# Kernel tuning notes

Measured on AMD Instinct MI355X. Metric: run time of the kernel, lower is better.

## Reference

```python
import jax, jax.numpy as jnp
import numpy as np

D_MODEL = 1024
NHEAD = 16
HEAD_DIM = D_MODEL // NHEAD
SF_THRESHOLD = 4.0
SF_LEVELS = 8
SF_STEP = SF_THRESHOLD / SF_LEVELS  # 0.5
EPS = 1e-6


def sfn(x):
    # Scale-and-Fire neuron: quantize activations to multiples of SF_STEP,
    # clipped to +/- num_levels, with straight-through estimator.
    q = jnp.clip(jnp.round(x / SF_STEP), -SF_LEVELS, SF_LEVELS) * SF_STEP
    return x + jax.lax.stop_gradient(q - x)


def qk_norm(x, g):
    # RMS-normalize over the head_dim (last axis) with learnable gain g [Dh].
    rms = jnp.sqrt(jnp.mean(x * x, axis=-1, keepdims=True) + EPS)
    return (x / rms) * g


def setup_inputs() -> dict:
    key = jax.random.key(0)
    ks = jax.random.split(key, 10)
    B, L, D = 2, 2048, D_MODEL
    s = 1.0 / np.sqrt(D)
    return {
        "x": jax.random.normal(ks[0], (B, L, D), dtype=jnp.float32),
        "Wq": jax.random.normal(ks[1], (D, D), dtype=jnp.float32) * s,
        "bq": jnp.zeros((D,), dtype=jnp.float32),
        "Wk": jax.random.normal(ks[2], (D, D), dtype=jnp.float32) * s,
        "bk": jnp.zeros((D,), dtype=jnp.float32),
        "Wv": jax.random.normal(ks[3], (D, D), dtype=jnp.float32) * s,
        "bv": jnp.zeros((D,), dtype=jnp.float32),
        "Wo": jax.random.normal(ks[4], (D, D), dtype=jnp.float32) * s,
        "bo": jnp.zeros((D,), dtype=jnp.float32),
        "gq": jnp.ones((HEAD_DIM,), dtype=jnp.float32),
        "gk": jnp.ones((HEAD_DIM,), dtype=jnp.float32),
    }


def reference(x, Wq, bq, Wk, bk, Wv, bv, Wo, bo, gq, gk):
    B, L, D = x.shape
    H, Dh = NHEAD, HEAD_DIM
    scale = Dh ** (-0.5)

    q = sfn(x @ Wq.T + bq)
    k = sfn(x @ Wk.T + bk)
    v = sfn(x @ Wv.T + bv)

    # [B, L, H, Dh] -> [B, H, L, Dh]
    q = q.reshape(B, L, H, Dh).transpose(0, 2, 1, 3)
    k = k.reshape(B, L, H, Dh).transpose(0, 2, 1, 3)
    v = v.reshape(B, L, H, Dh).transpose(0, 2, 1, 3)

    q = qk_norm(q, gq)
    k = qk_norm(k, gk)

    scores = jnp.einsum('bhqd,bhkd->bhqk', q, k) * scale
    probs = jax.nn.softmax(scores, axis=-1)  # dropout is identity (eval)
    out = jnp.einsum('bhqk,bhkd->bhqd', probs, v)
    out = out.transpose(0, 2, 1, 3).reshape(B, L, D)
    return out @ Wo.T + bo
```

## Files before the change

### kernel.cpp

```cpp
#include <hip/hip_runtime.h>
#include <math.h>


typedef __bf16 bf16;
typedef bf16 bf16x4 __attribute__((ext_vector_type(4)));
typedef bf16 bf16x8 __attribute__((ext_vector_type(8)));
typedef float f32x4 __attribute__((ext_vector_type(4)));

#define LOG2E 1.4426950408889634f
#define MFMA16 __builtin_amdgcn_mfma_f32_16x16x32_bf16
#define S_WAITV(N) asm volatile("s_waitcnt vmcnt(" #N ")" ::: "memory")

__device__ __forceinline__ void bar() {
  asm volatile("" ::: "memory");
  __builtin_amdgcn_s_barrier();
  asm volatile("" ::: "memory");
}

__device__ __forceinline__ float sfn_f(float x) {
  return fminf(fmaxf(rintf(x + x), -8.0f), 8.0f) * 0.5f;
}

__device__ __forceinline__ void gload16(const bf16* g, bf16* l) {
  __builtin_amdgcn_global_load_lds((const __attribute__((address_space(1))) void*)g,
                                   (__attribute__((address_space(3))) void*)l, 16, 0, 0);
}


__global__ __launch_bounds__(256) void prep_x_kernel(const float* __restrict__ x,
                                                     bf16* __restrict__ ax) {
  int idx = blockIdx.x * 256 + threadIdx.x;
  int m  = idx >> 8;
  int kc = (idx & 255) << 2;
  const float4 v = *(const float4*)(x + (size_t)m * 1024 + kc);
  bf16 h0 = (bf16)v.x, h1 = (bf16)v.y, h2 = (bf16)v.z, h3 = (bf16)v.w;
  bf16 l0 = (bf16)(v.x - (float)h0), l1 = (bf16)(v.y - (float)h1),
       l2 = (bf16)(v.z - (float)h2), l3 = (bf16)(v.w - (float)h3);
  bf16x4 hv = {h0, h1, h2, h3};
  bf16x4 lv = {l0, l1, l2, l3};
  bf16* p = ax + (size_t)m * 3072 + kc;
  *(bf16x4*)(p)        = hv;
  *(bf16x4*)(p + 1024) = lv;
  *(bf16x4*)(p + 2048) = hv;
}

__global__ __launch_bounds__(256) void prep_w_kernel(const float* __restrict__ Wq,
                                                     const float* __restrict__ Wk,
                                                     const float* __restrict__ Wv,
                                                     bf16* __restrict__ wc) {
  int idx = blockIdx.x * 256 + threadIdx.x;
  int mat = idx >> 18;
  int r   = idx & 262143;
  int n   = r >> 8;
  int kc  = (r & 255) << 2;
  const float* W = (mat == 0) ? Wq : ((mat == 1) ? Wk : Wv);
  const float4 v = *(const float4*)(W + (size_t)n * 1024 + kc);
  bf16 h0 = (bf16)v.x, h1 = (bf16)v.y, h2 = (bf16)v.z, h3 = (bf16)v.w;
  bf16 l0 = (bf16)(v.x - (float)h0), l1 = (bf16)(v.y - (float)h1),
       l2 = (bf16)(v.z - (float)h2), l3 = (bf16)(v.w - (float)h3);
  bf16x4 hv = {h0, h1, h2, h3};
  bf16x4 lv = {l0, l1, l2, l3};
  bf16* p = wc + (size_t)(mat * 1024 + n) * 3072 + kc;
  *(bf16x4*)(p)        = hv;
  *(bf16x4*)(p + 1024) = hv;
  *(bf16x4*)(p + 2048) = lv;
}

__global__ __launch_bounds__(256) void prep_wo_kernel(const float* __restrict__ Wo,
                                                      bf16* __restrict__ wob) {
  int idx = blockIdx.x * 256 + threadIdx.x;
  const float4 v = *(const float4*)(Wo + (size_t)idx * 4);
  bf16x4 hv = {(bf16)v.x, (bf16)v.y, (bf16)v.z, (bf16)v.w};
  *(bf16x4*)(wob + (size_t)idx * 4) = hv;
}


__global__ __launch_bounds__(512, 2) void gemm_qkv_kernel(
    const bf16* __restrict__ A, const bf16* __restrict__ Bm,
    const float* __restrict__ b0, const float* __restrict__ b1,
    const float* __restrict__ b2, const float* __restrict__ g0,
    const float* __restrict__ g1, bf16* __restrict__ qn, bf16* __restrict__ kn,
    bf16* __restrict__ vt) {
  constexpr int K = 3072, NT = 48;
  __shared__ bf16 lds[2][4][128 * 64];
  const int tid  = threadIdx.x;
  const int wave = tid >> 6;
  const int lane = tid & 63;
  const int lm   = lane & 15;
  const int kg   = lane >> 4;
  const int wm   = wave >> 2;
  const int wn   = wave & 3;
  const int lid     = blockIdx.x;
  const int logical = (lid & 7) * 24 + (lid >> 3);
  const int m0 = (logical / 12) << 8;
  const int n0 = (logical % 12) << 8;

  const bf16* Abase = A  + (size_t)m0 * K;
  const bf16* Bbase = Bm + (size_t)n0 * K;

  auto stageHalf = [&](int buf, int half, const bf16* base, int kt) {
#pragma unroll
    for (int j = 0; j < 2; ++j) {
      const int c    = j * 512 + tid;
      const int row  = c >> 3;
      const int col8 = (c & 7) ^ (row & 7);
      gload16(base + (size_t)row * K + kt + col8 * 8, &lds[buf][half][c * 8]);
    }
  };

  f32x4 acc[8][4] = {};
  const int bHalf = 2 + (wn >> 1);
  const int bRow  = (wn & 1) << 6;
  const int sw    = lm & 7;

  stageHalf(0, 0, Abase, 0);
  stageHalf(0, 1, Abase + (size_t)128 * K, 0);
  stageHalf(0, 2, Bbase, 0);
  stageHalf(0, 3, Bbase + (size_t)128 * K, 0);
  stageHalf(1, 0, Abase, 64);
  stageHalf(1, 1, Abase + (size_t)128 * K, 64);
  S_WAITV(4);
  bar();

  for (int t = 0; t < NT; ++t) {
    const int cur = t & 1, nxt = cur ^ 1;
    const int kt1 = (t + 1) << 6;
    bf16x8 a[4][2], p01[2][2], p23[2][2];
#pragma unroll
    for (int r = 0; r < 4; ++r)
#pragma unroll
      for (int kk = 0; kk < 2; ++kk)
        a[r][kk] = *(const bf16x8*)&lds[cur][wm][(16 * r + lm) * 64 + (((kk << 2) + kg) ^ sw) * 8];
#pragma unroll
    for (int c = 0; c < 2; ++c)
#pragma unroll
      for (int kk = 0; kk < 2; ++kk)
        p01[c][kk] = *(const bf16x8*)&lds[cur][bHalf][(bRow + 16 * c + lm) * 64 + (((kk << 2) + kg) ^ sw) * 8];
    if (t + 1 < NT) stageHalf(nxt, 2, Bbase, kt1);
    bar();
    __builtin_amdgcn_s_setprio(1);
#pragma unroll
    for (int r = 0; r < 4; ++r)
#pragma unroll
      for (int c = 0; c < 2; ++c)
#pragma unroll
        for (int kk = 0; kk < 2; ++kk)
          acc[r][c] = MFMA16(a[r][kk], p01[c][kk], acc[r][c], 0, 0, 0);
    __builtin_amdgcn_s_setprio(0);
    bar();
#pragma unroll
    for (int c = 0; c < 2; ++c)
#pragma unroll
      for (int kk = 0; kk < 2; ++kk)
        p23[c][kk] = *(const bf16x8*)&lds[cur][bHalf][(bRow + 16 * (c + 2) + lm) * 64 + (((kk << 2) + kg) ^ sw) * 8];
    if (t + 1 < NT) stageHalf(nxt, 3, Bbase + (size_t)128 * K, kt1);
    bar();
    __builtin_amdgcn_s_setprio(1);
#pragma unroll
    for (int r = 0; r < 4; ++r)
#pragma unroll
      for (int c = 0; c < 2; ++c)
#pragma unroll
        for (int kk = 0; kk < 2; ++kk)
          acc[r][c + 2] = MFMA16(a[r][kk], p23[c][kk], acc[r][c + 2], 0, 0, 0);
    __builtin_amdgcn_s_setprio(0);
    bar();
#pragma unroll
    for (int r = 0; r < 4; ++r)
#pragma unroll
      for (int kk = 0; kk < 2; ++kk)
        a[r][kk] = *(const bf16x8*)&lds[cur][wm][(64 + 16 * r + lm) * 64 + (((kk << 2) + kg) ^ sw) * 8];
    bar();
    __builtin_amdgcn_s_setprio(1);
#pragma unroll
    for (int r = 0; r < 4; ++r)
#pragma unroll
      for (int c = 0; c < 2; ++c)
#pragma unroll
        for (int kk = 0; kk < 2; ++kk)
          acc[4 + r][c + 2] = MFMA16(a[r][kk], p23[c][kk], acc[4 + r][c + 2], 0, 0, 0);
    __builtin_amdgcn_s_setprio(0);
    bar();
    if (t + 2 < NT) {
      const int kt2 = (t + 2) << 6;
      stageHalf(cur, 0, Abase, kt2);
      stageHalf(cur, 1, Abase + (size_t)128 * K, kt2);
      S_WAITV(4);
    } else {
      S_WAITV(0);
    }
    bar();
    __builtin_amdgcn_s_setprio(1);
#pragma unroll
    for (int r = 0; r < 4; ++r)
#pragma unroll
      for (int c = 0; c < 2; ++c)
#pragma unroll
        for (int kk = 0; kk < 2; ++kk)
          acc[4 + r][c] = MFMA16(a[r][kk], p01[c][kk], acc[4 + r][c], 0, 0, 0);
    __builtin_amdgcn_s_setprio(0);
    bar();
  }

  const int ncb = n0 + (wn << 6);
  const int mat = ncb >> 10;
  const int nin = ncb & 1023;
  const int hh  = nin >> 6;
  const float* bias = (mat == 0) ? b0 : ((mat == 1) ? b1 : b2);
  float bvals[4];
#pragma unroll
  for (int c = 0; c < 4; ++c) bvals[c] = bias[nin + 16 * c + lm];

  if (mat < 2) {
    const float* gain = (mat == 0) ? g0 : g1;
    bf16* dst = (mat == 0) ? qn : kn;
    float gv[4];
#pragma unroll
    for (int c = 0; c < 4; ++c) gv[c] = gain[16 * c + lm];
#pragma unroll
    for (int r = 0; r < 8; ++r) {
      float y[4][4];
      float ss[4] = {0.f, 0.f, 0.f, 0.f};
#pragma unroll
      for (int c = 0; c < 4; ++c)
#pragma unroll
        for (int g = 0; g < 4; ++g) {
          float tq = sfn_f(acc[r][c][g] + bvals[c]);
          y[c][g] = tq;
          ss[g] += tq * tq;
        }
#pragma unroll
      for (int g = 0; g < 4; ++g) {
        float s = ss[g];
        s += __shfl_xor(s, 1);
        s += __shfl_xor(s, 2);
        s += __shfl_xor(s, 4);
        s += __shfl_xor(s, 8);
        ss[g] = 1.0f / sqrtf(s * (1.0f / 64.0f) + 1e-6f);
      }
      const int mbase = m0 + (wm << 7) + 16 * r + 4 * kg;
      const int bb = mbase >> 11;
      const int ll = mbase & 2047;
#pragma unroll
      for (int g = 0; g < 4; ++g) {
        bf16* rowp = dst + ((size_t)(bb * 16 + hh) * 2048 + (ll + g)) * 64;
#pragma unroll
        for (int c = 0; c < 4; ++c)
          rowp[16 * c + lm] = (bf16)(y[c][g] * ss[g] * gv[c]);
      }
    }
  } else {
#pragma unroll
    for (int r = 0; r < 8; ++r) {
      const int mbase = m0 + (wm << 7) + 16 * r + 4 * kg;
      const int bb = mbase >> 11;
      const int ll = mbase & 2047;
#pragma unroll
      for (int c = 0; c < 4; ++c) {
        bf16x4 pk;
#pragma unroll
        for (int g = 0; g < 4; ++g)
          pk[g] = (bf16)sfn_f(acc[r][c][g] + bvals[c]);
        *(bf16x4*)(vt + ((size_t)(bb * 16 + hh) * 64 + 16 * c + lm) * 2048 + ll) = pk;
      }
    }
  }
}


__global__ __launch_bounds__(256, 3) void gemm_o_kernel(
    const bf16* __restrict__ A, const bf16* __restrict__ Bm, int K,
    const float* __restrict__ b0, float* __restrict__ outf) {
  __shared__ bf16 sA[128 * 32];
  __shared__ bf16 sB[128 * 32];
  const int tid  = threadIdx.x;
  const int wave = tid >> 6;
  const int lane = tid & 63;
  const int lm   = lane & 15;
  const int kg   = lane >> 4;
  const int nbx = gridDim.x;
  const int lid = blockIdx.x + nbx * blockIdx.y;
  const int cpx = (nbx << 5) >> 3;
  const int logical = (lid & 7) * cpx + (lid >> 3);
  const int m0 = (logical / nbx) << 7;
  const int n0 = (logical % nbx) << 7;
  const int wm = (wave >> 1) << 6;
  const int wn = (wave & 1) << 6;

  f32x4 acc[4][4] = {};

  for (int kt = 0; kt < K; kt += 32) {
    __syncthreads();
#pragma unroll
    for (int j = 0; j < 2; ++j) {
      const int i   = wave * 128 + j * 64 + lane;
      const int row = i >> 2;
      const int kc  = (i & 3) << 3;
      gload16(A  + (size_t)(m0 + row) * K + kt + kc, sA + i * 8);
      gload16(Bm + (size_t)(n0 + row) * K + kt + kc, sB + i * 8);
    }
    __syncthreads();
    bf16x8 af[4], bfv[4];
#pragma unroll
    for (int r = 0; r < 4; ++r)
      af[r] = *(const bf16x8*)(sA + (wm + 16 * r + lm) * 32 + kg * 8);
#pragma unroll
    for (int c = 0; c < 4; ++c)
      bfv[c] = *(const bf16x8*)(sB + (wn + 16 * c + lm) * 32 + kg * 8);
#pragma unroll
    for (int r = 0; r < 4; ++r)
#pragma unroll
      for (int c = 0; c < 4; ++c)
        acc[r][c] = MFMA16(af[r], bfv[c], acc[r][c], 0, 0, 0);
  }

  float bvals[4];
#pragma unroll
  for (int c = 0; c < 4; ++c) bvals[c] = b0[n0 + wn + 16 * c + lm];
#pragma unroll
  for (int r = 0; r < 4; ++r) {
    const int mr = m0 + wm + 16 * r + 4 * kg;
#pragma unroll
    for (int c = 0; c < 4; ++c) {
      const int nc = n0 + wn + 16 * c + lm;
#pragma unroll
      for (int g = 0; g < 4; ++g)
        outf[(size_t)(mr + g) * 1024 + nc] = acc[r][c][g] + bvals[c];
    }
  }
}


__global__ __launch_bounds__(256, 3) void attn_kernel(const bf16* __restrict__ qn,
                                                      const bf16* __restrict__ kn,
                                                      const bf16* __restrict__ vt,
                                                      bf16* __restrict__ ao) {
  __shared__ bf16 sK[2][64 * 64];
  __shared__ bf16 sV[2][64 * 64];
  __shared__ bf16 sP[4][2][16 * 72];
  const int tid  = threadIdx.x;
  const int wave = tid >> 6;
  const int lane = tid & 63;
  const int lm   = lane & 15;
  const int kg   = lane >> 4;
  const int lid     = blockIdx.x + (blockIdx.y << 4);
  const int logical = ((lid & 7) << 6) | (lid >> 3);
  const int qblk    = logical & 15;
  const int bh      = logical >> 4;
  const int q0      = (qblk << 7) + (wave << 5);
  const bf16* qb = qn + (size_t)bh * 2048 * 64;
  const bf16* kb = kn + (size_t)bh * 2048 * 64;
  const bf16* vb = vt + (size_t)bh * 64 * 2048;

  const float C1 = 0.125f * LOG2E;
  const float C2 = -8.0f * LOG2E;

  const int srow7 = lane >> 3;
  const int scl   = (lane & 7) ^ srow7;
  auto stageK = [&](int buf, int kt) {
#pragma unroll
    for (int j = 0; j < 2; ++j) {
      const int ci  = wave * 2 + j;
      const int row = ci * 8 + srow7;
      gload16(kb + (size_t)(kt + row) * 64 + scl * 8, &sK[buf][ci * 512]);
    }
  };
  auto stageV = [&](int buf, int kt) {
#pragma unroll
    for (int j = 0; j < 2; ++j) {
      const int ci  = wave * 2 + j;
      const int row = ci * 8 + srow7;
      gload16(vb + (size_t)row * 2048 + kt + scl * 8, &sV[buf][ci * 512]);
    }
  };

  bf16x8 qf[2][2];
#pragma unroll
  for (int c = 0; c < 2; ++c)
#pragma unroll
    for (int dh = 0; dh < 2; ++dh)
      qf[c][dh] = *(const bf16x8*)(qb + (size_t)(q0 + 16 * c + lm) * 64 + dh * 32 + kg * 8);

  f32x4 o[4][2] = {};
  float lrun[2] = {0.f, 0.f};

  stageK(0, 0);
  stageV(0, 0);
  S_WAITV(0);
  bar();

  const int a7 = lm & 7;
  for (int t = 0; t < 32; ++t) {
    const int cur = t & 1, nxt = cur ^ 1;
    const int ktn = (t + 1) << 6;
    if (t < 31) stageK(nxt, ktn);

    bf16x8 ka[4][2];
#pragma unroll
    for (int rb = 0; rb < 4; ++rb)
#pragma unroll
      for (int dh = 0; dh < 2; ++dh)
        ka[rb][dh] = *(const bf16x8*)(&sK[cur][(16 * rb + lm) * 64 + ((dh * 4 + kg) ^ a7) * 8]);

    f32x4 s[4][2] = {};
    __builtin_amdgcn_s_setprio(1);
#pragma unroll
    for (int rb = 0; rb < 4; ++rb)
#pragma unroll
      for (int c = 0; c < 2; ++c)
#pragma unroll
        for (int dh = 0; dh < 2; ++dh)
          s[rb][c] = MFMA16(ka[rb][dh], qf[c][dh], s[rb][c], 0, 0, 0);
    __builtin_amdgcn_s_setprio(0);

    if (t < 31) stageV(nxt, ktn);

#pragma unroll
    for (int c = 0; c < 2; ++c)
#pragma unroll
      for (int rb = 0; rb < 4; ++rb) {
        bf16x4 pk;
#pragma unroll
        for (int g = 0; g < 4; ++g) {
          float p = __builtin_amdgcn_exp2f(fmaf(s[rb][c][g], C1, C2));
          lrun[c] += p;
          pk[g] = (bf16)p;
        }
        *(bf16x4*)(&sP[wave][c][lm * 72 + 16 * rb + 4 * kg]) = pk;
      }
    bf16x8 pb[2][2];
#pragma unroll
    for (int c = 0; c < 2; ++c)
#pragma unroll
      for (int kh = 0; kh < 2; ++kh)
        pb[c][kh] = *(const bf16x8*)(&sP[wave][c][lm * 72 + kh * 32 + kg * 8]);

    if (t < 31) { S_WAITV(4); } else { S_WAITV(0); }
    bar();

    bf16x8 va[4][2];
#pragma unroll
    for (int rbd = 0; rbd < 4; ++rbd)
#pragma unroll
      for (int kh = 0; kh < 2; ++kh)
        va[rbd][kh] = *(const bf16x8*)(&sV[cur][(16 * rbd + lm) * 64 + ((kh * 4 + kg) ^ a7) * 8]);

    __builtin_amdgcn_s_setprio(1);
#pragma unroll
    for (int rbd = 0; rbd < 4; ++rbd)
#pragma unroll
      for (int c = 0; c < 2; ++c)
#pragma unroll
        for (int kh = 0; kh < 2; ++kh)
          o[rbd][c] = MFMA16(va[rbd][kh], pb[c][kh], o[rbd][c], 0, 0, 0);
    __builtin_amdgcn_s_setprio(0);

    if (t < 31) {
      S_WAITV(2);
      bar();
    }
  }

  const int bb = bh >> 4;
  const int hh = bh & 15;
#pragma unroll
  for (int c = 0; c < 2; ++c) {
    float l = lrun[c];
    l += __shfl_xor(l, 16);
    l += __shfl_xor(l, 32);
    const float inv = 1.0f / l;
    const int q = q0 + 16 * c + lm;
    bf16* rowp = ao + (size_t)(bb * 2048 + q) * 1024 + hh * 64;
#pragma unroll
    for (int rbd = 0; rbd < 4; ++rbd) {
      bf16x4 pk;
#pragma unroll
      for (int g = 0; g < 4; ++g)
        pk[g] = (bf16)(o[rbd][c][g] * inv);
      *(bf16x4*)(rowp + 16 * rbd + 4 * kg) = pk;
    }
  }
}


extern "C" void kernel_launch(void* const* d_in, const int* in_sizes, int n_in,
                              void* d_out, int out_size, void* d_ws, size_t ws_size,
                              hipStream_t stream) {
  const float* x  = (const float*)d_in[0];
  const float* Wq = (const float*)d_in[1];
  const float* bq = (const float*)d_in[2];
  const float* Wk = (const float*)d_in[3];
  const float* bk = (const float*)d_in[4];
  const float* Wv = (const float*)d_in[5];
  const float* bv = (const float*)d_in[6];
  const float* Wo = (const float*)d_in[7];
  const float* bo = (const float*)d_in[8];
  const float* gq = (const float*)d_in[9];
  const float* gk = (const float*)d_in[10];
  float* out = (float*)d_out;

  char* ws = (char*)d_ws;
  bf16* ax   = (bf16*)(ws);
  bf16* wc   = (bf16*)(ws + 25165824);
  bf16* wob  = (bf16*)(ws + 44040192);
  bf16* qn   = (bf16*)(ws + 46137344);
  bf16* kn   = (bf16*)(ws + 54525952);
  bf16* vt   = (bf16*)(ws + 62914560);
  bf16* attn = (bf16*)(ws + 71303168);

  prep_x_kernel<<<dim3(4096), dim3(256), 0, stream>>>(x, ax);
  prep_w_kernel<<<dim3(3072), dim3(256), 0, stream>>>(Wq, Wk, Wv, wc);
  prep_wo_kernel<<<dim3(1024), dim3(256), 0, stream>>>(Wo, wob);

  gemm_qkv_kernel<<<dim3(192), dim3(512), 0, stream>>>(
      ax, wc, bq, bk, bv, gq, gk, qn, kn, vt);

  attn_kernel<<<dim3(16, 32), dim3(256), 0, stream>>>(qn, kn, vt, attn);

  gemm_o_kernel<<<dim3(8, 32), dim3(256), 0, stream>>>(
      attn, wob, 1024, bo, out);
}
```

Baseline: 260.4 us.

## Retile QKV GEMM to 256x192 over 256 blocks and software-pipeline attention QK/PV

The QKV projection GEMM moves from 256x256 tiles on 192 blocks to 256x192 tiles on 256 blocks. Each wave now owns 32 rows by 192 columns, and the LDS staging and the fused epilogue are restructured to match. The goal is better CU occupancy on the 256-CU part without a partial last wave of blocks. The attention kernel is software-pipelined: the QK^T scores for tile t+1 are computed while the PV MFMAs for tile t run. K uses triple buffering and there is one barrier per iteration. The changes cost more registers and more complex scheduling, plus a per-wave P buffer that relies on lgkmcnt waits for ordering.

Measured after the change: 247.6 us. 1.05x faster.

```diff
diff --git a/kernel.cpp b/kernel.cpp
--- a/kernel.cpp
+++ b/kernel.cpp
@@ -82,109 +82,106 @@
     const float* __restrict__ g1, bf16* __restrict__ qn, bf16* __restrict__ kn,
     bf16* __restrict__ vt) {
   constexpr int K = 3072, NT = 48;
-  __shared__ bf16 lds[2][4][128 * 64];
+  __shared__ bf16 lds[2][28672];
   const int tid  = threadIdx.x;
   const int wave = tid >> 6;
   const int lane = tid & 63;
   const int lm   = lane & 15;
   const int kg   = lane >> 4;
-  const int wm   = wave >> 2;
-  const int wn   = wave & 3;
   const int lid     = blockIdx.x;
-  const int logical = (lid & 7) * 24 + (lid >> 3);
-  const int m0 = (logical / 12) << 8;
-  const int n0 = (logical % 12) << 8;
-
-  const bf16* Abase = A  + (size_t)m0 * K;
-  const bf16* Bbase = Bm + (size_t)n0 * K;
-
-  auto stageHalf = [&](int buf, int half, const bf16* base, int kt) {
+  const int logical = ((lid & 7) << 5) | (lid >> 3);
+  const int m0 = (logical >> 4) << 8;
+  const int n0 = (logical & 15) * 192;
+
+  auto stageA = [&](int buf, int half, int kt) {
 #pragma unroll
     for (int j = 0; j < 2; ++j) {
       const int c    = j * 512 + tid;
       const int row  = c >> 3;
       const int col8 = (c & 7) ^ (row & 7);
-      gload16(base + (size_t)row * K + kt + col8 * 8, &lds[buf][half][c * 8]);
+      gload16(A + (size_t)(m0 + half * 128 + row) * K + kt + col8 * 8,
+              &lds[buf][half * 8192 + c * 8]);
     }
   };
-
-  f32x4 acc[8][4] = {};
-  const int bHalf = 2 + (wn >> 1);
-  const int bRow  = (wn & 1) << 6;
+  auto stageB = [&](int buf, int ch, int kt) {
+    const int row  = tid >> 3;
+    const int col8 = (tid & 7) ^ (row & 7);
+    gload16(Bm + (size_t)(n0 + ch * 64 + row) * K + kt + col8 * 8,
+            &lds[buf][16384 + ch * 4096 + tid * 8]);
+  };
+
   const int sw    = lm & 7;
-
-  stageHalf(0, 0, Abase, 0);
-  stageHalf(0, 1, Abase + (size_t)128 * K, 0);
-  stageHalf(0, 2, Bbase, 0);
-  stageHalf(0, 3, Bbase + (size_t)128 * K, 0);
-  stageHalf(1, 0, Abase, 64);
-  stageHalf(1, 1, Abase + (size_t)128 * K, 64);
+  const int arow  = (wave << 5) + lm;
+  auto rdA = [&](int buf, int r, int kk) -> bf16x8 {
+    const int row = arow + 16 * r;
+    return *(const bf16x8*)&lds[buf][(row >> 7) * 8192 + (row & 127) * 64 +
+                                     (((kk << 2) + kg) ^ sw) * 8];
+  };
+  auto rdB = [&](int buf, int c, int kk) -> bf16x8 {
+    const int col = 16 * c + lm;
+    return *(const bf16x8*)&lds[buf][16384 + (col >> 6) * 4096 + (col & 63) * 64 +
+                                     (((kk << 2) + kg) ^ sw) * 8];
+  };
+
+  f32x4 acc[2][12] = {};
+
+  stageA(0, 0, 0); stageA(0, 1, 0);
+  stageB(0, 0, 0); stageB(0, 1, 0); stageB(0, 2, 0);
+  stageA(1, 0, 64); stageA(1, 1, 64);
   S_WAITV(4);
   bar();
 
   for (int t = 0; t < NT; ++t) {
     const int cur = t & 1, nxt = cur ^ 1;
-    const int kt1 = (t + 1) << 6;
-    bf16x8 a[4][2], p01[2][2], p23[2][2];
-#pragma unroll
-    for (int r = 0; r < 4; ++r)
+    const int kt1 = (t + 1) << 6, kt2 = (t + 2) << 6;
+    bf16x8 a[2][2], bv[6];
+#pragma unroll
+    for (int r = 0; r < 2; ++r)
 #pragma unroll
       for (int kk = 0; kk < 2; ++kk)
-        a[r][kk] = *(const bf16x8*)&lds[cur][wm][(16 * r + lm) * 64 + (((kk << 2) + kg) ^ sw) * 8];
-#pragma unroll
-    for (int c = 0; c < 2; ++c)
-#pragma unroll
-      for (int kk = 0; kk < 2; ++kk)
-        p01[c][kk] = *(const bf16x8*)&lds[cur][bHalf][(bRow + 16 * c + lm) * 64 + (((kk << 2) + kg) ^ sw) * 8];
-    if (t + 1 < NT) stageHalf(nxt, 2, Bbase, kt1);
+        a[r][kk] = rdA(cur, r, kk);
+#pragma unroll
+    for (int c = 0; c < 6; ++c) bv[c] = rdB(cur, c, 0);
+    if (t + 1 < NT) stageB(nxt, 0, kt1);
     bar();
     __builtin_amdgcn_s_setprio(1);
 #pragma unroll
-    for (int r = 0; r < 4; ++r)
-#pragma unroll
-      for (int c = 0; c < 2; ++c)
-#pragma unroll
-        for (int kk = 0; kk < 2; ++kk)
-          acc[r][c] = MFMA16(a[r][kk], p01[c][kk], acc[r][c], 0, 0, 0);
+    for (int r = 0; r < 2; ++r)
+#pragma unroll
+      for (int c = 0; c < 6; ++c)
+        acc[r][c] = MFMA16(a[r][0], bv[c], acc[r][c], 0, 0, 0);
     __builtin_amdgcn_s_setprio(0);
     bar();
-#pragma unroll
-    for (int c = 0; c < 2; ++c)
-#pragma unroll
-      for (int kk = 0; kk < 2; ++kk)
-        p23[c][kk] = *(const bf16x8*)&lds[cur][bHalf][(bRow + 16 * (c + 2) + lm) * 64 + (((kk << 2) + kg) ^ sw) * 8];
-    if (t + 1 < NT) stageHalf(nxt, 3, Bbase + (size_t)128 * K, kt1);
+    bf16x8 bw[6];
+#pragma unroll
+    for (int c = 0; c < 6; ++c) bw[c] = rdB(cur, c + 6, 0);
+    if (t + 1 < NT) { stageB(nxt, 1, kt1); stageB(nxt, 2, kt1); }
     bar();
     __builtin_amdgcn_s_setprio(1);
 #pragma unroll
-    for (int r = 0; r < 4; ++r)
-#pragma unroll
-      for (int c = 0; c < 2; ++c)
-#pragma unroll
-        for (int kk = 0; kk < 2; ++kk)
-          acc[r][c + 2] = MFMA16(a[r][kk], p23[c][kk], acc[r][c + 2], 0, 0, 0);
+    for (int r = 0; r < 2; ++r)
+#pragma unroll
+      for (int c = 0; c < 6; ++c)
+        acc[r][c + 6] = MFMA16(a[r][0], bw[c], acc[r][c + 6], 0, 0, 0);
     __builtin_amdgcn_s_setprio(0);
     bar();
-#pragma unroll
-    for (int r = 0; r < 4; ++r)
-#pragma unroll
-      for (int kk = 0; kk < 2; ++kk)
-        a[r][kk] = *(const bf16x8*)&lds[cur][wm][(64 + 16 * r + lm) * 64 + (((kk << 2) + kg) ^ sw) * 8];
+    bf16x8 bx[6];
+#pragma unroll
+    for (int c = 0; c < 6; ++c) bx[c] = rdB(cur, c, 1);
     bar();
     __builtin_amdgcn_s_setprio(1);
 #pragma unroll
-    for (int r = 0; r < 4; ++r)
-#pragma unroll
-      for (int c = 0; c < 2; ++c)
-#pragma unroll
-        for (int kk = 0; kk < 2; ++kk)
-          acc[4 + r][c + 2] = MFMA16(a[r][kk], p23[c][kk], acc[4 + r][c + 2], 0, 0, 0);
+    for (int r = 0; r < 2; ++r)
+#pragma unroll
+      for (int c = 0; c < 6; ++c)
+        acc[r][c] = MFMA16(a[r][1], bx[c], acc[r][c], 0, 0, 0);
     __builtin_amdgcn_s_setprio(0);
     bar();
+    bf16x8 by[6];
+#pragma unroll
+    for (int c = 0; c < 6; ++c) by[c] = rdB(cur, c + 6, 1);
     if (t + 2 < NT) {
-      const int kt2 = (t + 2) << 6;
-      stageHalf(cur, 0, Abase, kt2);
-      stageHalf(cur, 1, Abase + (size_t)128 * K, kt2);
+      stageA(cur, 0, kt2); stageA(cur, 1, kt2);
       S_WAITV(4);
     } else {
       S_WAITV(0);
@@ -192,76 +189,77 @@
     bar();
     __builtin_amdgcn_s_setprio(1);
 #pragma unroll
-    for (int r = 0; r < 4; ++r)
-#pragma unroll
-      for (int c = 0; c < 2; ++c)
-#pragma unroll
-        for (int kk = 0; kk < 2; ++kk)
-          acc[4 + r][c] = MFMA16(a[r][kk], p01[c][kk], acc[4 + r][c], 0, 0, 0);
+    for (int r = 0; r < 2; ++r)
+#pragma unroll
+      for (int c = 0; c < 6; ++c)
+        acc[r][c + 6] = MFMA16(a[r][1], by[c], acc[r][c + 6], 0, 0, 0);
     __builtin_amdgcn_s_setprio(0);
     bar();
   }
 
-  const int ncb = n0 + (wn << 6);
-  const int mat = ncb >> 10;
-  const int nin = ncb & 1023;
-  const int hh  = nin >> 6;
-  const float* bias = (mat == 0) ? b0 : ((mat == 1) ? b1 : b2);
-  float bvals[4];
-#pragma unroll
-  for (int c = 0; c < 4; ++c) bvals[c] = bias[nin + 16 * c + lm];
-
-  if (mat < 2) {
-    const float* gain = (mat == 0) ? g0 : g1;
-    bf16* dst = (mat == 0) ? qn : kn;
-    float gv[4];
-#pragma unroll
-    for (int c = 0; c < 4; ++c) gv[c] = gain[16 * c + lm];
-#pragma unroll
-    for (int r = 0; r < 8; ++r) {
-      float y[4][4];
-      float ss[4] = {0.f, 0.f, 0.f, 0.f};
-#pragma unroll
-      for (int c = 0; c < 4; ++c)
+#pragma unroll
+  for (int h = 0; h < 3; ++h) {
+    const int gcol = n0 + (h << 6);
+    const int mat  = gcol >> 10;
+    const int cb   = gcol & 1023;
+    const int hh   = cb >> 6;
+    const float* bias = (mat == 0) ? b0 : ((mat == 1) ? b1 : b2);
+    float bvals[4];
+#pragma unroll
+    for (int j = 0; j < 4; ++j) bvals[j] = bias[cb + 16 * j + lm];
+
+    if (mat < 2) {
+      const float* gain = (mat == 0) ? g0 : g1;
+      bf16* dst = (mat == 0) ? qn : kn;
+      float gv[4];
+#pragma unroll
+      for (int j = 0; j < 4; ++j) gv[j] = gain[16 * j + lm];
+#pragma unroll
+      for (int r = 0; r < 2; ++r) {
+        float y[4][4];
+        float ss[4] = {0.f, 0.f, 0.f, 0.f};
+#pragma unroll
+        for (int j = 0; j < 4; ++j)
+#pragma unroll
+          for (int g = 0; g < 4; ++g) {
+            float tq = sfn_f(acc[r][4 * h + j][g] + bvals[j]);
+            y[j][g] = tq;
+            ss[g] += tq * tq;
+          }
 #pragma unroll
         for (int g = 0; g < 4; ++g) {
-          float tq = sfn_f(acc[r][c][g] + bvals[c]);
-          y[c][g] = tq;
-          ss[g] += tq * tq;
+          float s = ss[g];
+          s += __shfl_xor(s, 1);
+          s += __shfl_xor(s, 2);
+          s += __shfl_xor(s, 4);
+          s += __shfl_xor(s, 8);
+          ss[g] = 1.0f / sqrtf(s * (1.0f / 64.0f) + 1e-6f);
         }
-#pragma unroll
-      for (int g = 0; g < 4; ++g) {
-        float s = ss[g];
-        s += __shfl_xor(s, 1);
-        s += __shfl_xor(s, 2);
-        s += __shfl_xor(s, 4);
-        s += __shfl_xor(s, 8);
-        ss[g] = 1.0f / sqrtf(s * (1.0f / 64.0f) + 1e-6f);
+        const int mbase = m0 + (wave << 5) + 16 * r + 4 * kg;
+        const int bb = mbase >> 11;
+        const int ll = mbase & 2047;
+#pragma unroll
+        for (int g = 0; g < 4; ++g) {
+          bf16* rowp = dst + ((size_t)(bb * 16 + hh) * 2048 + (ll + g)) * 64;
+#pragma unroll
+          for (int j = 0; j < 4; ++j)
+            rowp[16 * j + lm] = (bf16)(y[j][g] * ss[g] * gv[j]);
+        }
       }
-      const int mbase = m0 + (wm << 7) + 16 * r + 4 * kg;
-      const int bb = mbase >> 11;
-      const int ll = mbase & 2047;
-#pragma unroll
-      for (int g = 0; g < 4; ++g) {
-        bf16* rowp = dst + ((size_t)(bb * 16 + hh) * 2048 + (ll + g)) * 64;
-#pragma unroll
-        for (int c = 0; c < 4; ++c)
-          rowp[16 * c + lm] = (bf16)(y[c][g] * ss[g] * gv[c]);
-      }
-    }
-  } else {
-#pragma unroll
-    for (int r = 0; r < 8; ++r) {
-      const int mbase = m0 + (wm << 7) + 16 * r + 4 * kg;
-      const int bb = mbase >> 11;
-      const int ll = mbase & 2047;
-#pragma unroll
-      for (int c = 0; c < 4; ++c) {
-        bf16x4 pk;
-#pragma unroll
-        for (int g = 0; g < 4; ++g)
-          pk[g] = (bf16)sfn_f(acc[r][c][g] + bvals[c]);
-        *(bf16x4*)(vt + ((size_t)(bb * 16 + hh) * 64 + 16 * c + lm) * 2048 + ll) = pk;
+    } else {
+#pragma unroll
+      for (int r = 0; r < 2; ++r) {
+        const int mbase = m0 + (wave << 5) + 16 * r + 4 * kg;
+        const int bb = mbase >> 11;
+        const int ll = mbase & 2047;
+#pragma unroll
+        for (int j = 0; j < 4; ++j) {
+          bf16x4 pk;
+#pragma unroll
+          for (int g = 0; g < 4; ++g)
+            pk[g] = (bf16)sfn_f(acc[r][4 * h + j][g] + bvals[j]);
+          *(bf16x4*)(vt + ((size_t)(bb * 16 + hh) * 64 + 16 * j + lm) * 2048 + ll) = pk;
+        }
       }
     }
   }
@@ -335,9 +333,9 @@
                                                       const bf16* __restrict__ kn,
                                                       const bf16* __restrict__ vt,
                                                       bf16* __restrict__ ao) {
-  __shared__ bf16 sK[2][64 * 64];
+  __shared__ bf16 sK[3][64 * 64];
   __shared__ bf16 sV[2][64 * 64];
-  __shared__ bf16 sP[4][2][16 * 72];
+  __shared__ bf16 sP[4][16 * 72];
   const int tid  = threadIdx.x;
   const int wave = tid >> 6;
   const int lane = tid & 63;
@@ -383,27 +381,22 @@
 
   f32x4 o[4][2] = {};
   float lrun[2] = {0.f, 0.f};
-
+  bf16x8 pb[2][2];
+  const int a7 = lm & 7;
+
+  stageV(0, 0);
   stageK(0, 0);
-  stageV(0, 0);
+  stageK(1, 64);
   S_WAITV(0);
   bar();
-
-  const int a7 = lm & 7;
-  for (int t = 0; t < 32; ++t) {
-    const int cur = t & 1, nxt = cur ^ 1;
-    const int ktn = (t + 1) << 6;
-    if (t < 31) stageK(nxt, ktn);
-
+  {
     bf16x8 ka[4][2];
 #pragma unroll
     for (int rb = 0; rb < 4; ++rb)
 #pragma unroll
       for (int dh = 0; dh < 2; ++dh)
-        ka[rb][dh] = *(const bf16x8*)(&sK[cur][(16 * rb + lm) * 64 + ((dh * 4 + kg) ^ a7) * 8]);
-
+        ka[rb][dh] = *(const bf16x8*)(&sK[0][(16 * rb + lm) * 64 + ((dh * 4 + kg) ^ a7) * 8]);
     f32x4 s[4][2] = {};
-    __builtin_amdgcn_s_setprio(1);
 #pragma unroll
     for (int rb = 0; rb < 4; ++rb)
 #pragma unroll
@@ -411,12 +404,8 @@
 #pragma unroll
         for (int dh = 0; dh < 2; ++dh)
           s[rb][c] = MFMA16(ka[rb][dh], qf[c][dh], s[rb][c], 0, 0, 0);
-    __builtin_amdgcn_s_setprio(0);
-
-    if (t < 31) stageV(nxt, ktn);
-
-#pragma unroll
-    for (int c = 0; c < 2; ++c)
+#pragma unroll
+    for (int c = 0; c < 2; ++c) {
 #pragma unroll
       for (int rb = 0; rb < 4; ++rb) {
         bf16x4 pk;
@@ -426,39 +415,88 @@
           lrun[c] += p;
           pk[g] = (bf16)p;
         }
-        *(bf16x4*)(&sP[wave][c][lm * 72 + 16 * rb + 4 * kg]) = pk;
+        *(bf16x4*)(&sP[wave][lm * 72 + 16 * rb + 4 * kg]) = pk;
       }
-    bf16x8 pb[2][2];
-#pragma unroll
-    for (int c = 0; c < 2; ++c)
+      asm volatile("s_waitcnt lgkmcnt(0)" ::: "memory");
 #pragma unroll
       for (int kh = 0; kh < 2; ++kh)
-        pb[c][kh] = *(const bf16x8*)(&sP[wave][c][lm * 72 + kh * 32 + kg * 8]);
-
-    if (t < 31) { S_WAITV(4); } else { S_WAITV(0); }
-    bar();
-
-    bf16x8 va[4][2];
-#pragma unroll
-    for (int rbd = 0; rbd < 4; ++rbd)
-#pragma unroll
-      for (int kh = 0; kh < 2; ++kh)
-        va[rbd][kh] = *(const bf16x8*)(&sV[cur][(16 * rbd + lm) * 64 + ((kh * 4 + kg) ^ a7) * 8]);
-
-    __builtin_amdgcn_s_setprio(1);
-#pragma unroll
-    for (int rbd = 0; rbd < 4; ++rbd)
-#pragma unroll
-      for (int c = 0; c < 2; ++c)
+        pb[c][kh] = *(const bf16x8*)(&sP[wave][lm * 72 + kh * 32 + kg * 8]);
+    }
+  }
+  stageK(2, 128);
+  bar();
+
+  for (int t = 0; t < 32; ++t) {
+    const int vcur = t & 1;
+    if (t + 1 < 32) stageV((t + 1) & 1, (t + 1) << 6);
+    if (t + 3 < 32) stageK((t + 3) % 3, (t + 3) << 6);
+
+    f32x4 s[4][2];
+    if (t + 1 < 32) {
+      const bf16* kbuf = sK[(t + 1) % 3];
+      bf16x8 ka[4][2];
+#pragma unroll
+      for (int rb = 0; rb < 4; ++rb)
+#pragma unroll
+        for (int dh = 0; dh < 2; ++dh)
+          ka[rb][dh] = *(const bf16x8*)(&kbuf[(16 * rb + lm) * 64 + ((dh * 4 + kg) ^ a7) * 8]);
+#pragma unroll
+      for (int rb = 0; rb < 4; ++rb)
+#pragma unroll
+        for (int c = 0; c < 2; ++c)
+          s[rb][c] = f32x4{0.f, 0.f, 0.f, 0.f};
+      __builtin_amdgcn_s_setprio(1);
+#pragma unroll
+      for (int rb = 0; rb < 4; ++rb)
+#pragma unroll
+        for (int c = 0; c < 2; ++c)
+#pragma unroll
+          for (int dh = 0; dh < 2; ++dh)
+            s[rb][c] = MFMA16(ka[rb][dh], qf[c][dh], s[rb][c], 0, 0, 0);
+      __builtin_amdgcn_s_setprio(0);
+    }
+
+    {
+      bf16x8 va[4][2];
+#pragma unroll
+      for (int rbd = 0; rbd < 4; ++rbd)
 #pragma unroll
         for (int kh = 0; kh < 2; ++kh)
-          o[rbd][c] = MFMA16(va[rbd][kh], pb[c][kh], o[rbd][c], 0, 0, 0);
-    __builtin_amdgcn_s_setprio(0);
-
-    if (t < 31) {
-      S_WAITV(2);
-      bar();
-    }
+          va[rbd][kh] = *(const bf16x8*)(&sV[vcur][(16 * rbd + lm) * 64 + ((kh * 4 + kg) ^ a7) * 8]);
+      __builtin_amdgcn_s_setprio(1);
+#pragma unroll
+      for (int rbd = 0; rbd < 4; ++rbd)
+#pragma unroll
+        for (int c = 0; c < 2; ++c)
+#pragma unroll
+          for (int kh = 0; kh < 2; ++kh)
+            o[rbd][c] = MFMA16(va[rbd][kh], pb[c][kh], o[rbd][c], 0, 0, 0);
+      __builtin_amdgcn_s_setprio(0);
+    }
+
+    if (t + 1 < 32) {
+#pragma unroll
+      for (int c = 0; c < 2; ++c) {
+#pragma unroll
+        for (int rb = 0; rb < 4; ++rb) {
+          bf16x4 pk;
+#pragma unroll
+          for (int g = 0; g < 4; ++g) {
+            float p = __builtin_amdgcn_exp2f(fmaf(s[rb][c][g], C1, C2));
+            lrun[c] += p;
+            pk[g] = (bf16)p;
+          }
+          *(bf16x4*)(&sP[wave][lm * 72 + 16 * rb + 4 * kg]) = pk;
+        }
+        asm volatile("s_waitcnt lgkmcnt(0)" ::: "memory");
+#pragma unroll
+        for (int kh = 0; kh < 2; ++kh)
+          pb[c][kh] = *(const bf16x8*)(&sP[wave][lm * 72 + kh * 32 + kg * 8]);
+      }
+    }
+
+    if (t + 3 < 32) { S_WAITV(2); } else { S_WAITV(0); }
+    bar();
   }
 
   const int bb = bh >> 4;
@@ -512,7 +550,7 @@
   prep_w_kernel<<<dim3(3072), dim3(256), 0, stream>>>(Wq, Wk, Wv, wc);
   prep_wo_kernel<<<dim3(1024), dim3(256), 0, stream>>>(Wo, wob);
 
-  gemm_qkv_kernel<<<dim3(192), dim3(512), 0, stream>>>(
+  gemm_qkv_kernel<<<dim3(256), dim3(512), 0, stream>>>(
       ax, wc, bq, bk, bv, gq, gk, qn, kn, vt);
 
   attn_kernel<<<dim3(16, 32), dim3(256), 0, stream>>>(qn, kn, vt, attn);
```
